# Kernel optimization log

Measured on AMD Instinct MI355X. Metric: run time of the kernel, lower is better.

Reference implementation:

```python
import jax, jax.numpy as jnp
import numpy as np

E, B, T = 7, 50, 100               # ensemble (network_size), no_batches=50, time blocks
D, A, L, H, C = 128, 32, 256, 1024, 128  # data, action, latent, hidden, context sizes
H_STEP = 0.1                        # (t1 - t0) / T == dt -> one SDE step per block


def setup_inputs() -> dict:
    key = jax.random.key(0)
    ks = iter(jax.random.split(key, 64))
    def nrm(shape, scale=1.0):
        return jax.random.normal(next(ks), shape, jnp.float32) * scale
    def ens(i, o):
        s = 1.0 / np.sqrt(i)
        return nrm((E, i, o), s), nrm((E, o), s)
    def lin(i, o):
        s = 1.0 / np.sqrt(i)
        return nrm((i, o), s), nrm((o,), s)
    inp = {}
    inp["enc_w1"], inp["enc_b1"] = ens(D, H)
    inp["enc_w2"], inp["enc_b2"] = ens(H, H)
    inp["enc_w3"], inp["enc_b3"] = ens(H, C)
    inp["qz0_w"], inp["qz0_b"] = ens(C, 2 * L)
    inp["act_w"], inp["act_b"] = ens(L + A + D, L)
    inp["proj_w1"], inp["proj_b1"] = ens(L, H)
    inp["proj_w2"], inp["proj_b2"] = ens(H, H)
    inp["proj_w3"], inp["proj_b3"] = ens(H, D)
    inp["f_w1"], inp["f_b1"] = lin(L, H)
    inp["f_w2"], inp["f_b2"] = lin(H, H)
    inp["f_w3"], inp["f_b3"] = lin(H, L)
    inp["h_w1"], inp["h_b1"] = lin(L, H)
    inp["h_w2"], inp["h_b2"] = lin(H, H)
    inp["h_w3"], inp["h_b3"] = lin(H, L)
    # per-latent-dim g nets: Linear(1,H) -> ReLU -> Linear(H,1), stacked over L dims
    inp["g_w1"] = nrm((L, H), 0.2)
    inp["g_b1"] = nrm((L, H), 0.2)
    inp["g_w2"] = nrm((L, H), 0.2 / np.sqrt(H))
    inp["g_b2"] = 0.5 + nrm((L,), 0.01)   # keep diffusion bounded away from 0
    inp["pz0_mean"] = jnp.zeros((E, 1, L), jnp.float32)
    inp["pz0_logstd"] = jnp.zeros((E, 1, L), jnp.float32)
    inp["xs"] = nrm((E, T * B, D))
    inp["actions"] = nrm((E, T * B, A))
    inp["eps_z0"] = nrm((T, E, B, L))      # torch.randn_like noise for z0 reparam
    inp["dw_noise"] = nrm((T, E * B, L))   # Brownian increment noise (unit std)
    return inp


def reference(enc_w1, enc_b1, enc_w2, enc_b2, enc_w3, enc_b3,
              qz0_w, qz0_b, act_w, act_b,
              proj_w1, proj_b1, proj_w2, proj_b2, proj_w3, proj_b3,
              f_w1, f_b1, f_w2, f_b2, f_w3, f_b3,
              h_w1, h_b1, h_w2, h_b2, h_w3, h_b3,
              g_w1, g_b1, g_w2, g_b2,
              pz0_mean, pz0_logstd,
              xs, actions, eps_z0, dw_noise):
    def ens_lin(x, w, b):  # EnsembleFC: bmm + bias
        return jnp.einsum('ebi,eio->ebo', x, w) + b[:, None, :]

    def encoder(x):
        x = jax.nn.relu(ens_lin(x, enc_w1, enc_b1))
        x = jax.nn.relu(ens_lin(x, enc_w2, enc_b2))
        return ens_lin(x, enc_w3, enc_b3)

    def projector(z):
        z = jnp.tanh(ens_lin(z, proj_w1, proj_b1))
        z = jnp.tanh(ens_lin(z, proj_w2, proj_b2))
        return ens_lin(z, proj_w3, proj_b3)

    def mlp(y, w1, b1, w2, b2, w3, b3):  # Linear-ReLU-Linear-Tanh-Linear
        y = jax.nn.relu(y @ w1 + b1)
        y = jnp.tanh(y @ w2 + b2)
        return y @ w3 + b3

    def g_fn(y):  # vectorized per-dim tiny MLPs: y (N, L) -> (N, L)
        hh = jax.nn.relu(y[:, :, None] * g_w1[None] + g_b1[None])  # (N, L, H)
        return jnp.sum(hh * g_w2[None], axis=-1) + g_b2

    xs_t = jnp.moveaxis(xs.reshape(E, T, B, D), 1, 0)        # (T, E, B, D)
    act_t = jnp.moveaxis(actions.reshape(E, T, B, A), 1, 0)  # (T, E, B, A)
    sqrt_h = jnp.sqrt(jnp.float32(H_STEP))

    def step(carry, inps):
        zs_last, i = carry
        x_i, a_i, eps_i, dw_i = inps
        ctx = encoder(x_i)                                  # (E, B, C)
        q = ens_lin(ctx, qz0_w, qz0_b)                      # (E, B, 2L)
        qm, ql = q[..., :L], q[..., L:]
        z0 = qm + jnp.exp(ql) * eps_i
        z_in = jnp.where(i == 0, z0, zs_last)               # first step uses z0
        lad = jnp.concatenate([z_in, a_i, x_i], axis=2)
        z = ens_lin(lad, act_w, act_b).reshape(E * B, L)
        # one SDE step with logqp (f: posterior drift, h: prior drift, g: diffusion)
        fv = mlp(z, f_w1, f_b1, f_w2, f_b2, f_w3, f_b3)
        hv = mlp(z, h_w1, h_b1, h_w2, h_b2, h_w3, h_b3)
        gv = g_fn(z)
        u = (fv - hv) / gv
        lr = 0.5 * jnp.sum(u * u, axis=-1) * H_STEP         # (E*B,) log-ratio increment
        z_new = z + fv * H_STEP + gv * (sqrt_h * dw_i)
        zs_new = z_new.reshape(E, B, L)
        xm = projector(zs_new)                              # (E, B, D)
        # KL(q(z0) || p(z0)) for diagonal Gaussians
        kl = (pz0_logstd - ql) \
             + (jnp.exp(2.0 * ql) + (qm - pz0_mean) ** 2) / (2.0 * jnp.exp(2.0 * pz0_logstd)) \
             - 0.5
        logqp0 = kl.sum(axis=2).mean(axis=1)                # (E,)
        lr_mean = lr.reshape(E, B).mean(axis=1)             # (E,)
        return (zs_new, i + 1), (lr_mean, logqp0, xm)

    init = (jnp.zeros((E, B, L), xs.dtype), jnp.int32(0))
    (_, _), (lrm, lq0, xms) = jax.lax.scan(step, init, (xs_t, act_t, eps_z0, dw_noise))
    logqp_path = lrm.sum(axis=0) + lq0.sum(axis=0)          # (E,)
    predicted_xs = jnp.moveaxis(xms, 0, 1).reshape(E, T * B, D)
    return logqp_path, predicted_xs
```

## Files before the change

kernel.cpp:

```cpp
#include <hip/hip_runtime.h>
#include <hip/hip_bf16.h>
#include <math.h>

#define E_ 7
#define B_ 50
#define T_ 100
#define D_ 128
#define A_ 32
#define L_ 256
#define H_ 1024
#define C_ 128
#define LAD_ 416
#define EB_ 350
#define TB_ 5000
#define SQRTH 0.31622776601683794f

typedef __attribute__((ext_vector_type(8))) short s8v;
typedef __attribute__((ext_vector_type(4))) float f32x4;
typedef __hip_bfloat16 bf16;

struct BG {
  const bf16* A[8];
  const bf16* W[8];
  const float* bias[8];
  float* Cf[8];
  bf16* Cb[8];
};

template<int BM, int ACT, int OUT>
__global__ __launch_bounds__(256)
void bgemm(BG g, int M, int K, int lda, int ldw, int ldc) {
  __shared__ short As[BM * 64];
  __shared__ short Ws[128 * 64];
  const short* Ap = (const short*)g.A[blockIdx.z];
  const short* Wp = (const short*)g.W[blockIdx.z];
  const int bm = blockIdx.x * BM, bn = blockIdx.y * 128;
  const int tid = threadIdx.x;
  const int wv = tid >> 6, lane = tid & 63;
  const int wm0 = (wv >> 1) * (BM / 2), wn0 = (wv & 1) * 64;
  const int l15 = lane & 15, l4 = lane >> 4;
  constexpr int FM = BM / 32;
  constexpr int AI = BM / 32;
  f32x4 acc[FM][4] = {};
  for (int k0 = 0; k0 < K; k0 += 64) {
    s8v av[AI], wvv[4];
#pragma unroll
    for (int i = 0; i < AI; ++i) {
      const int c = tid + i * 256, r = c >> 3, ck = c & 7;
      s8v v = {};
      if (bm + r < M) v = *(const s8v*)(Ap + (size_t)(bm + r) * lda + k0 + ck * 8);
      av[i] = v;
// ... 60 lines not shown
  }
}

__global__ __launch_bounds__(256)
void cvtT_kernel(const float* __restrict__ src, bf16* __restrict__ dst,
                 int K, int N, long ss, long ds) {
  __shared__ float t[32][33];
  src += (size_t)blockIdx.z * ss;
  dst += (size_t)blockIdx.z * ds;
  const int n0 = blockIdx.x * 32, k0 = blockIdx.y * 32;
  const int tx = threadIdx.x & 31, ty = threadIdx.x >> 5;
#pragma unroll
  for (int i = 0; i < 4; ++i)
    t[ty + 8 * i][tx] = src[(size_t)(k0 + ty + 8 * i) * N + n0 + tx];
  __syncthreads();
#pragma unroll
  for (int i = 0; i < 4; ++i)
    dst[(size_t)(n0 + ty + 8 * i) * K + k0 + tx] = __float2bfloat16(t[tx][ty + 8 * i]);
}

struct B4 { bf16 a, b, c, d; };
__global__ __launch_bounds__(256)
void cvt_kernel(const float* __restrict__ s, bf16* __restrict__ d, int n4) {
  const int i = blockIdx.x * 256 + threadIdx.x;
  if (i < n4) {
    const float4 v = ((const float4*)s)[i];
    B4 o = {__float2bfloat16(v.x), __float2bfloat16(v.y),
            __float2bfloat16(v.z), __float2bfloat16(v.w)};
    ((B4*)d)[i] = o;
  }
}

__global__ __launch_bounds__(256)
void act_gemm(const float* __restrict__ zin, int zin_estride,
              const float* __restrict__ actions, const float* __restrict__ xs,
              const float* __restrict__ act_w, const float* __restrict__ act_b,
              float* __restrict__ zout, bf16* __restrict__ zout_bf, int t) {
  __shared__ float As[16][68];
  __shared__ float Bs[16][64];
  const int tid = threadIdx.x;
  const int e = blockIdx.y;
  const int bn = blockIdx.x * 64;
  const int tm = (tid >> 4) << 2;
  const int tn = (tid & 15) << 2;
  const int am = tid >> 2;
  const int ak = (tid & 3) << 2;
  const int bk = tid >> 4;
  const int bn4 = (tid & 15) << 2;
  const float* W = act_w + (size_t)e * LAD_ * L_;
  const float* zin_e = zin + (size_t)e * zin_estride;
  float acc[4][4] = {};
  for (int k0 = 0; k0 < LAD_; k0 += 16) {
    float4 av = make_float4(0.f, 0.f, 0.f, 0.f);
    const int k = k0 + ak;
    if (am < B_) {
      if (k < L_)
        av = *(const float4*)(zin_e + (size_t)am * L_ + k);
      else if (k < L_ + A_)
        av = *(const float4*)(actions + ((size_t)e * TB_ + (size_t)t * B_ + am) * A_ + (k - L_));
      else
        av = *(const float4*)(xs + ((size_t)e * TB_ + (size_t)t * B_ + am) * D_ + (k - L_ - A_));
    }
    const float4 wv = *(const float4*)(W + (size_t)(k0 + bk) * L_ + (bn + bn4));
    __syncthreads();
    As[ak + 0][am] = av.x; As[ak + 1][am] = av.y;
    As[ak + 2][am] = av.z; As[ak + 3][am] = av.w;
    *(float4*)&Bs[bk][bn4] = wv;
    __syncthreads();
#pragma unroll
    for (int kk = 0; kk < 16; ++kk) {
      const float4 a4 = *(const float4*)&As[kk][tm];
      const float4 b4 = *(const float4*)&Bs[kk][tn];
      const float ar[4] = {a4.x, a4.y, a4.z, a4.w};
      const float br[4] = {b4.x, b4.y, b4.z, b4.w};
#pragma unroll
      for (int i = 0; i < 4; ++i)
#pragma unroll
        for (int j = 0; j < 4; ++j)
          acc[i][j] = fmaf(ar[i], br[j], acc[i][j]);
    }
  }
#pragma unroll
  for (int i = 0; i < 4; ++i) {
    const int m = tm + i;
    if (m < B_) {
#pragma unroll
      for (int j = 0; j < 4; ++j) {
        const float v = acc[i][j] + act_b[(size_t)e * L_ + bn + tn + j];
        const size_t idx = ((size_t)e * B_ + m) * L_ + (bn + tn + j);
        zout[idx] = v;
        zout_bf[idx] = __float2bfloat16(v);
      }
    }
  }
}

__global__ __launch_bounds__(256)
void qkl_kernel(const float* __restrict__ ctx, int rows, int row_off, int ctx_estride,
                const float* __restrict__ qw, const float* __restrict__ qb,
                const float* __restrict__ pm, const float* __restrict__ pl,
                const float* __restrict__ eps0, float* __restrict__ z0,
                float* __restrict__ logqp) {
  __shared__ float cx[16][128];
  __shared__ float red[16];
  const int e = blockIdx.y;
  const int r0 = blockIdx.x * 16;
  const int tid = threadIdx.x;
  {
    const int r = tid >> 4, c = (tid & 15) * 8;
    float4 v0 = make_float4(0.f, 0.f, 0.f, 0.f), v1 = v0;
    if (r0 + r < rows) {
      const float* src = ctx + (size_t)e * ctx_estride + (size_t)(r0 + r) * C_ + c;
      v0 = *(const float4*)src;
      v1 = *(const float4*)(src + 4);
    }
    *(float4*)&cx[r][c] = v0;
    *(float4*)&cx[r][c + 4] = v1;
  }
  if (tid < 16) red[tid] = 0.f;
  __syncthreads();
  const int j = tid;
  const float* w = qw + (size_t)e * C_ * 512;
  float am_[16] = {};
  float al_[16] = {};
  for (int k0 = 0; k0 < C_; k0 += 4) {
    float wm[4], wl[4];
#pragma unroll
    for (int q = 0; q < 4; ++q) {
      wm[q] = w[(size_t)(k0 + q) * 512 + j];
      wl[q] = w[(size_t)(k0 + q) * 512 + 256 + j];
    }
#pragma unroll
    for (int r = 0; r < 16; ++r) {
      const float4 cv = *(const float4*)&cx[r][k0];
      const float cc[4] = {cv.x, cv.y, cv.z, cv.w};
#pragma unroll
      for (int q = 0; q < 4; ++q) {
        am_[r] = fmaf(cc[q], wm[q], am_[r]);
        al_[r] = fmaf(cc[q], wl[q], al_[r]);
      }
    }
  }
  const float qbm = qb[(size_t)e * 512 + j];
  const float qbl = qb[(size_t)e * 512 + 256 + j];
  const float pmv = pm[(size_t)e * L_ + j];
  const float plv = pl[(size_t)e * L_ + j];
  const float inv2e = 0.5f * expf(-2.f * plv);
#pragma unroll
  for (int r = 0; r < 16; ++r) {
    float kl = 0.f;
    if (r0 + r < rows) {
      const float qm_ = am_[r] + qbm;
      const float ql_ = al_[r] + qbl;
      const float dm = qm_ - pmv;
      kl = plv - ql_ + (expf(2.f * ql_) + dm * dm) * inv2e - 0.5f;
      const int gi = row_off + r0 + r;
      if (gi < B_) {
        const size_t zi = ((size_t)e * B_ + gi) * L_ + j;
        z0[zi] = qm_ + expf(ql_) * eps0[zi];
      }
    }
    for (int off = 32; off; off >>= 1) kl += __shfl_xor(kl, off, 64);
    if ((tid & 63) == 0) atomicAdd(&red[r], kl);
  }
  __syncthreads();
  if (tid < 16 && r0 + tid < rows) atomicAdd(&logqp[e], red[tid] * (1.0f / B_));
}

__global__ __launch_bounds__(64)
void g_kernel(const float* __restrict__ z, const float* __restrict__ gw1,
              const float* __restrict__ gb1, const float* __restrict__ gw2,
              const float* __restrict__ gb2, float* __restrict__ gv) {
  const int l = blockIdx.x;
  const int r0 = blockIdx.y * 44;
  const int rend = (r0 + 44 < EB_) ? (r0 + 44) : EB_;
  const int lane = threadIdx.x;
  float w1[16], b1[16], w2[16];
#pragma unroll
  for (int i = 0; i < 16; ++i) {
    const int h = lane + i * 64;
    w1[i] = gw1[(size_t)l * H_ + h];
    b1[i] = gb1[(size_t)l * H_ + h];
    w2[i] = gw2[(size_t)l * H_ + h];
  }
  const float g2 = gb2[l];
  for (int r = r0; r < rend; ++r) {
    const float zv = z[(size_t)r * L_ + l];
    float acc = 0.f;
#pragma unroll
    for (int i = 0; i < 16; ++i) {
      float hh = fmaf(zv, w1[i], b1[i]);
      hh = fmaxf(hh, 0.f);
      acc = fmaf(hh, w2[i], acc);
    }
    for (int off = 32; off; off >>= 1) acc += __shfl_xor(acc, off, 64);
    if (lane == 0) gv[(size_t)r * L_ + l] = acc + g2;
  }
}

__global__ __launch_bounds__(256)
void epi_kernel(const float* __restrict__ fvp, const float* __restrict__ fb3,
                const float* __restrict__ hb3, const float* __restrict__ gv,
                const float* __restrict__ z, const float* __restrict__ dw,
                float* __restrict__ zs_all, bf16* __restrict__ zs_bf,
                float* __restrict__ logqp, int t) {
  __shared__ float wsum[4];
  const int r = blockIdx.x;
  const int l = threadIdx.x;
  const int e = r / B_, b = r - e * B_;
  const size_t rl = (size_t)r * L_ + l;
  float fv = fb3[l], hv = hb3[l];
#pragma unroll
  for (int s = 0; s < 4; ++s) {
    fv += fvp[(size_t)s * EB_ * L_ + rl];
    hv += fvp[(size_t)(4 + s) * EB_ * L_ + rl];
  }
  const float gvv = gv[rl];
  const float u = (fv - hv) / gvv;
  float s_ = u * u;
  for (int off = 32; off; off >>= 1) s_ += __shfl_xor(s_, off, 64);
  if ((l & 63) == 0) wsum[l >> 6] = s_;
  __syncthreads();
  if (l == 0) {
    const float tot = wsum[0] + wsum[1] + wsum[2] + wsum[3];
    atomicAdd(&logqp[e], 0.5f * tot * 0.1f * (1.0f / B_));
  }
  const float znew = z[rl] + fv * 0.1f + gvv * (SQRTH * dw[(size_t)t * EB_ * L_ + rl]);
  const size_t oi = (((size_t)e * T_ + t) * B_ + b) * L_ + l;
  zs_all[oi] = znew;
  zs_bf[oi] = __float2bfloat16(znew);
}

__global__ void init_kernel(float* logqp) {
  if (threadIdx.x < E_) logqp[threadIdx.x] = 0.f;
}

extern "C" void kernel_launch(void* const* d_in, const int* in_sizes, int n_in,
                              void* d_out, int out_size, void* d_ws, size_t ws_size,
                              hipStream_t stream) {
  (void)in_sizes; (void)n_in; (void)out_size;
  const float* enc_w1 = (const float*)d_in[0];
  const float* enc_b1 = (const float*)d_in[1];
  const float* enc_w2 = (const float*)d_in[2];
  const float* enc_b2 = (const float*)d_in[3];
  const float* enc_w3 = (const float*)d_in[4];
  const float* enc_b3 = (const float*)d_in[5];
  const float* qz0_w  = (const float*)d_in[6];
  const float* qz0_b  = (const float*)d_in[7];
  const float* act_w  = (const float*)d_in[8];
  const float* act_b  = (const float*)d_in[9];
  const float* proj_w1 = (const float*)d_in[10];
  const float* proj_b1 = (const float*)d_in[11];
  const float* proj_w2 = (const float*)d_in[12];
  const float* proj_b2 = (const float*)d_in[13];
  const float* proj_w3 = (const float*)d_in[14];
  const float* proj_b3 = (const float*)d_in[15];
  const float* f_w1 = (const float*)d_in[16];
  const float* f_b1 = (const float*)d_in[17];
  const float* f_w2 = (const float*)d_in[18];
  const float* f_b2 = (const float*)d_in[19];
  const float* f_w3 = (const float*)d_in[20];
  const float* f_b3 = (const float*)d_in[21];
  const float* h_w1 = (const float*)d_in[22];
  const float* h_b1 = (const float*)d_in[23];
  const float* h_w2 = (const float*)d_in[24];
  const float* h_b2 = (const float*)d_in[25];
  const float* h_w3 = (const float*)d_in[26];
  const float* h_b3 = (const float*)d_in[27];
  const float* g_w1 = (const float*)d_in[28];
  const float* g_b1 = (const float*)d_in[29];
  const float* g_w2 = (const float*)d_in[30];
  const float* g_b2 = (const float*)d_in[31];
  const float* pz0_mean   = (const float*)d_in[32];
  const float* pz0_logstd = (const float*)d_in[33];
  const float* xs      = (const float*)d_in[34];
  const float* actions = (const float*)d_in[35];
  const float* eps_z0  = (const float*)d_in[36];
  const float* dw      = (const float*)d_in[37];

  float* out = (float*)d_out;
  float* logqp = out;
  float* pred = out + E_;

  char* base = (char*)d_ws;
  size_t off = 0;
  auto alloc = [&](size_t bytes) {
    void* p = base + off;
    off = (off + bytes + 255) & ~(size_t)255;
    return p;
  };
  float* zs_all = (float*)alloc((size_t)E_ * T_ * B_ * L_ * 4);
  bf16* zs_bf   = (bf16*)alloc((size_t)E_ * T_ * B_ * L_ * 2);
  float* z0     = (float*)alloc((size_t)E_ * B_ * L_ * 4);
  float* zbuf   = (float*)alloc((size_t)EB_ * L_ * 4);
  bf16* zbuf_bf = (bf16*)alloc((size_t)EB_ * L_ * 2);
  bf16* fh1     = (bf16*)alloc((size_t)2 * EB_ * H_ * 2);
  bf16* fh2     = (bf16*)alloc((size_t)2 * EB_ * H_ * 2);
  float* fvhvp  = (float*)alloc((size_t)8 * EB_ * L_ * 4);
  float* gvb    = (float*)alloc((size_t)EB_ * L_ * 4);
  bf16* xs_bf   = (bf16*)alloc((size_t)E_ * TB_ * D_ * 2);
  bf16* ew1T = (bf16*)alloc((size_t)E_ * D_ * H_ * 2);
  bf16* ew2T = (bf16*)alloc((size_t)E_ * H_ * H_ * 2);
  bf16* ew3T = (bf16*)alloc((size_t)E_ * H_ * C_ * 2);
  bf16* pw1T = (bf16*)alloc((size_t)E_ * L_ * H_ * 2);
  bf16* pw2T = (bf16*)alloc((size_t)E_ * H_ * H_ * 2);
  bf16* pw3T = (bf16*)alloc((size_t)E_ * H_ * D_ * 2);
  bf16* fw1T = (bf16*)alloc((size_t)L_ * H_ * 2);
  bf16* fw2T = (bf16*)alloc((size_t)H_ * H_ * 2);
  bf16* fw3T = (bf16*)alloc((size_t)H_ * L_ * 2);
  bf16* hw1T = (bf16*)alloc((size_t)L_ * H_ * 2);
  bf16* hw2T = (bf16*)alloc((size_t)H_ * H_ * 2);
  bf16* hw3T = (bf16*)alloc((size_t)H_ * L_ * 2);
  const size_t per_row = (size_t)E_ * (H_ * 2 * 2 + C_ * 4);
  size_t remain = (ws_size > off + 4096) ? (ws_size - off - 4096) : 0;
  int CH = (int)(remain / per_row);
  if (CH > 2500) CH = 2500;
  if (CH < 64) CH = 64;
  bf16* bufA = (bf16*)alloc((size_t)E_ * CH * H_ * 2);
  bf16* bufB = (bf16*)alloc((size_t)E_ * CH * H_ * 2);
  float* bufC = (float*)alloc((size_t)E_ * CH * C_ * 4);

  init_kernel<<<dim3(1), dim3(64), 0, stream>>>(logqp);

  const dim3 cb(256);
  cvt_kernel<<<dim3((E_ * TB_ * D_ / 4 + 255) / 256), cb, 0, stream>>>(xs, xs_bf, E_ * TB_ * D_ / 4);
  cvtT_kernel<<<dim3(H_ / 32, D_ / 32, E_), cb, 0, stream>>>(enc_w1, ew1T, D_, H_, (long)D_ * H_, (long)D_ * H_);
  cvtT_kernel<<<dim3(H_ / 32, H_ / 32, E_), cb, 0, stream>>>(enc_w2, ew2T, H_, H_, (long)H_ * H_, (long)H_ * H_);
  cvtT_kernel<<<dim3(C_ / 32, H_ / 32, E_), cb, 0, stream>>>(enc_w3, ew3T, H_, C_, (long)H_ * C_, (long)H_ * C_);
  cvtT_kernel<<<dim3(H_ / 32, L_ / 32, E_), cb, 0, stream>>>(proj_w1, pw1T, L_, H_, (long)L_ * H_, (long)L_ * H_);
  cvtT_kernel<<<dim3(H_ / 32, H_ / 32, E_), cb, 0, stream>>>(proj_w2, pw2T, H_, H_, (long)H_ * H_, (long)H_ * H_);
  cvtT_kernel<<<dim3(D_ / 32, H_ / 32, E_), cb, 0, stream>>>(proj_w3, pw3T, H_, D_, (long)H_ * D_, (long)H_ * D_);
  cvtT_kernel<<<dim3(H_ / 32, L_ / 32, 1), cb, 0, stream>>>(f_w1, fw1T, L_, H_, 0, 0);
  cvtT_kernel<<<dim3(H_ / 32, H_ / 32, 1), cb, 0, stream>>>(f_w2, fw2T, H_, H_, 0, 0);
  cvtT_kernel<<<dim3(L_ / 32, H_ / 32, 1), cb, 0, stream>>>(f_w3, fw3T, H_, L_, 0, 0);
  cvtT_kernel<<<dim3(H_ / 32, L_ / 32, 1), cb, 0, stream>>>(h_w1, hw1T, L_, H_, 0, 0);
  cvtT_kernel<<<dim3(H_ / 32, H_ / 32, 1), cb, 0, stream>>>(h_w2, hw2T, H_, H_, 0, 0);
  cvtT_kernel<<<dim3(L_ / 32, H_ / 32, 1), cb, 0, stream>>>(h_w3, hw3T, H_, L_, 0, 0);

  BG g;
  for (int c = 0; c < TB_; c += CH) {
    const int rows = (TB_ - c < CH) ? (TB_ - c) : CH;
    const int mt = (rows + 127) / 128;
    for (int e = 0; e < E_; ++e) {
      g.A[e] = xs_bf + ((size_t)e * TB_ + c) * D_;
      g.W[e] = ew1T + (size_t)e * D_ * H_;
      g.bias[e] = enc_b1 + (size_t)e * H_;
      g.Cb[e] = bufA + (size_t)e * CH * H_;
    }
    bgemm<128, 1, 1><<<dim3(mt, H_ / 128, E_), 256, 0, stream>>>(g, rows, D_, D_, D_, H_);
    for (int e = 0; e < E_; ++e) {
      g.A[e] = bufA + (size_t)e * CH * H_;
      g.W[e] = ew2T + (size_t)e * H_ * H_;
      g.bias[e] = enc_b2 + (size_t)e * H_;
      g.Cb[e] = bufB + (size_t)e * CH * H_;
    }
    bgemm<128, 1, 1><<<dim3(mt, H_ / 128, E_), 256, 0, stream>>>(g, rows, H_, H_, H_, H_);
    for (int e = 0; e < E_; ++e) {
      g.A[e] = bufB + (size_t)e * CH * H_;
      g.W[e] = ew3T + (size_t)e * H_ * C_;
      g.bias[e] = enc_b3 + (size_t)e * C_;
      g.Cf[e] = bufC + (size_t)e * CH * C_;
    }
    bgemm<128, 0, 0><<<dim3(mt, C_ / 128, E_), 256, 0, stream>>>(g, rows, H_, H_, H_, C_);
    qkl_kernel<<<dim3((rows + 15) / 16, E_), 256, 0, stream>>>(
        bufC, rows, c, CH * C_, qz0_w, qz0_b, pz0_mean, pz0_logstd, eps_z0, z0, logqp);
  }

  for (int t = 0; t < T_; ++t) {
    const float* zin;
    int zes;
    if (t == 0) { zin = z0; zes = B_ * L_; }
    else { zin = zs_all + (size_t)(t - 1) * B_ * L_; zes = T_ * B_ * L_; }
    act_gemm<<<dim3(L_ / 64, E_), 256, 0, stream>>>(zin, zes, actions, xs, act_w, act_b,
                                                    zbuf, zbuf_bf, t);
    g.A[0] = zbuf_bf; g.W[0] = fw1T; g.bias[0] = f_b1; g.Cb[0] = fh1;
    g.A[1] = zbuf_bf; g.W[1] = hw1T; g.bias[1] = h_b1; g.Cb[1] = fh1 + (size_t)EB_ * H_;
    bgemm<64, 1, 1><<<dim3(6, H_ / 128, 2), 256, 0, stream>>>(g, EB_, L_, L_, L_, H_);
    g.A[0] = fh1; g.W[0] = fw2T; g.bias[0] = f_b2; g.Cb[0] = fh2;
    g.A[1] = fh1 + (size_t)EB_ * H_; g.W[1] = hw2T; g.bias[1] = h_b2;
    g.Cb[1] = fh2 + (size_t)EB_ * H_;
    bgemm<64, 2, 1><<<dim3(6, H_ / 128, 2), 256, 0, stream>>>(g, EB_, H_, H_, H_, H_);
    for (int jj = 0; jj < 8; ++jj) {
      const int fb = jj >> 2, s = jj & 3;
      g.A[jj] = fh2 + (size_t)fb * EB_ * H_ + s * 256;
      g.W[jj] = (fb ? hw3T : fw3T) + s * 256;
      g.bias[jj] = nullptr;
      g.Cf[jj] = fvhvp + (size_t)jj * EB_ * L_;
    }
    bgemm<64, 0, 0><<<dim3(6, L_ / 128, 8), 256, 0, stream>>>(g, EB_, 256, H_, H_, L_);
    g_kernel<<<dim3(L_, 8), 64, 0, stream>>>(zbuf, g_w1, g_b1, g_w2, g_b2, gvb);
    epi_kernel<<<dim3(EB_), 256, 0, stream>>>(fvhvp, f_b3, h_b3, gvb, zbuf, dw,
                                              zs_all, zs_bf, logqp, t);
  }

  for (int c = 0; c < TB_; c += CH) {
    const int rows = (TB_ - c < CH) ? (TB_ - c) : CH;
    const int mt = (rows + 127) / 128;
    for (int e = 0; e < E_; ++e) {
      g.A[e] = zs_bf + ((size_t)e * T_ * B_ + c) * L_;
      g.W[e] = pw1T + (size_t)e * L_ * H_;
      g.bias[e] = proj_b1 + (size_t)e * H_;
      g.Cb[e] = bufA + (size_t)e * CH * H_;
    }
    bgemm<128, 2, 1><<<dim3(mt, H_ / 128, E_), 256, 0, stream>>>(g, rows, L_, L_, L_, H_);
    for (int e = 0; e < E_; ++e) {
      g.A[e] = bufA + (size_t)e * CH * H_;
      g.W[e] = pw2T + (size_t)e * H_ * H_;
      g.bias[e] = proj_b2 + (size_t)e * H_;
      g.Cb[e] = bufB + (size_t)e * CH * H_;
    }
    bgemm<128, 2, 1><<<dim3(mt, H_ / 128, E_), 256, 0, stream>>>(g, rows, H_, H_, H_, H_);
    for (int e = 0; e < E_; ++e) {
      g.A[e] = bufB + (size_t)e * CH * H_;
      g.W[e] = pw3T + (size_t)e * H_ * D_;
      g.bias[e] = proj_b3 + (size_t)e * D_;
      g.Cf[e] = pred + ((size_t)e * TB_ + c) * D_;
    }
    bgemm<128, 0, 0><<<dim3(mt, D_ / 128, E_), 256, 0, stream>>>(g, rows, H_, H_, H_, D_);
  }
}
```

Before: 11.16 ms.

## Fuse SDE time-step loop into one persistent cooperative kernel with grid barriers

```diff
diff --git a/kernel.cpp b/kernel.cpp
--- a/kernel.cpp
+++ b/kernel.cpp
@@ -10,13 +10,14 @@
 #define L_ 256
 #define H_ 1024
 #define C_ 128
-#define LAD_ 416
 #define EB_ 350
 #define TB_ 5000
 #define SQRTH 0.31622776601683794f
+#define NWG 256
 
 typedef __attribute__((ext_vector_type(8))) short s8v;
 typedef __attribute__((ext_vector_type(4))) float f32x4;
+typedef _Float16 f16x2 __attribute__((ext_vector_type(2)));
 typedef __hip_bfloat16 bf16;
 
 struct BG {
@@ -143,75 +144,50 @@
 }
 
 __global__ __launch_bounds__(256)
-void act_gemm(const float* __restrict__ zin, int zin_estride,
-              const float* __restrict__ actions, const float* __restrict__ xs,
-              const float* __restrict__ act_w, const float* __restrict__ act_b,
-              float* __restrict__ zout, bf16* __restrict__ zout_bf, int t) {
-  __shared__ float As[16][68];
-  __shared__ float Bs[16][64];
-  const int tid = threadIdx.x;
-  const int e = blockIdx.y;
-  const int bn = blockIdx.x * 64;
-  const int tm = (tid >> 4) << 2;
-  const int tn = (tid & 15) << 2;
-  const int am = tid >> 2;
-  const int ak = (tid & 3) << 2;
-  const int bk = tid >> 4;
-  const int bn4 = (tid & 15) << 2;
-  const float* W = act_w + (size_t)e * LAD_ * L_;
-  const float* zin_e = zin + (size_t)e * zin_estride;
-  float acc[4][4] = {};
-  for (int k0 = 0; k0 < LAD_; k0 += 16) {
-    float4 av = make_float4(0.f, 0.f, 0.f, 0.f);
-    const int k = k0 + ak;
-    if (am < B_) {
-      if (k < L_)
-        av = *(const float4*)(zin_e + (size_t)am * L_ + k);
-      else if (k < L_ + A_)
-        av = *(const float4*)(actions + ((size_t)e * TB_ + (size_t)t * B_ + am) * A_ + (k - L_));
-      else
-        av = *(const float4*)(xs + ((size_t)e * TB_ + (size_t)t * B_ + am) * D_ + (k - L_ - A_));
-    }
-    const float4 wv = *(const float4*)(W + (size_t)(k0 + bk) * L_ + (bn + bn4));
-    __syncthreads();
-    As[ak + 0][am] = av.x; As[ak + 1][am] = av.y;
-    As[ak + 2][am] = av.z; As[ak + 3][am] = av.w;
-    *(float4*)&Bs[bk][bn4] = wv;
-    __syncthreads();
-#pragma unroll
-    for (int kk = 0; kk < 16; ++kk) {
-      const float4 a4 = *(const float4*)&As[kk][tm];
-      const float4 b4 = *(const float4*)&Bs[kk][tn];
-      const float ar[4] = {a4.x, a4.y, a4.z, a4.w};
-      const float br[4] = {b4.x, b4.y, b4.z, b4.w};
-#pragma unroll
-      for (int i = 0; i < 4; ++i)
-#pragma unroll
-        for (int j = 0; j < 4; ++j)
-          acc[i][j] = fmaf(ar[i], br[j], acc[i][j]);
-    }
-  }
-#pragma unroll
-  for (int i = 0; i < 4; ++i) {
-    const int m = tm + i;
-    if (m < B_) {
-#pragma unroll
-      for (int j = 0; j < 4; ++j) {
-        const float v = acc[i][j] + act_b[(size_t)e * L_ + bn + tn + j];
-        const size_t idx = ((size_t)e * B_ + m) * L_ + (bn + tn + j);
-        zout[idx] = v;
-        zout_bf[idx] = __float2bfloat16(v);
-      }
-    }
-  }
+void ax_build(const float* __restrict__ actions, const float* __restrict__ xs,
+              bf16* __restrict__ dst) {
+  const int idx = blockIdx.x * 256 + threadIdx.x;
+  if (idx >= E_ * TB_ * 192) return;
+  const int k = idx % 192;
+  const int r = (idx / 192) % TB_;
+  const int e = idx / (192 * TB_);
+  float v = 0.f;
+  if (k < 32) v = actions[((size_t)e * TB_ + r) * A_ + k];
+  else if (k < 160) v = xs[((size_t)e * TB_ + r) * D_ + (k - 32)];
+  dst[idx] = __float2bfloat16(v);
+}
+
+__global__ __launch_bounds__(256)
+void waxT_build(const float* __restrict__ act_w, bf16* __restrict__ dst) {
+  const int idx = blockIdx.x * 256 + threadIdx.x;
+  if (idx >= E_ * 256 * 192) return;
+  const int k = idx % 192;
+  const int n = (idx / 192) % 256;
+  const int e = idx / (192 * 256);
+  float v = (k < 160) ? act_w[(size_t)e * 416 * 256 + (size_t)(256 + k) * 256 + n] : 0.f;
+  dst[idx] = __float2bfloat16(v);
+}
+
+__global__ __launch_bounds__(256)
+void wsplitT_build(const float* __restrict__ act_w, bf16* __restrict__ hi,
+                   bf16* __restrict__ lo) {
+  const int idx = blockIdx.x * 256 + threadIdx.x;
+  if (idx >= E_ * 256 * 256) return;
+  const int k = idx & 255;
+  const int n = (idx >> 8) & 255;
+  const int e = idx >> 16;
+  const float w = act_w[(size_t)e * 416 * 256 + (size_t)k * 256 + n];
+  const bf16 h = __float2bfloat16(w);
+  hi[idx] = h;
+  lo[idx] = __float2bfloat16(w - __bfloat162float(h));
 }
 
 __global__ __launch_bounds__(256)
 void qkl_kernel(const float* __restrict__ ctx, int rows, int row_off, int ctx_estride,
                 const float* __restrict__ qw, const float* __restrict__ qb,
                 const float* __restrict__ pm, const float* __restrict__ pl,
-                const float* __restrict__ eps0, float* __restrict__ z0,
-                float* __restrict__ logqp) {
+                const float* __restrict__ eps0, bf16* __restrict__ z0hi,
+                bf16* __restrict__ z0lo, float* __restrict__ logqp) {
   __shared__ float cx[16][128];
   __shared__ float red[16];
   const int e = blockIdx.y;
@@ -268,7 +244,10 @@
       const int gi = row_off + r0 + r;
       if (gi < B_) {
         const size_t zi = ((size_t)e * B_ + gi) * L_ + j;
-        z0[zi] = qm_ + expf(ql_) * eps0[zi];
+        const float z0 = qm_ + expf(ql_) * eps0[zi];
+        const bf16 h = __float2bfloat16(z0);
+        z0hi[zi] = h;
+        z0lo[zi] = __float2bfloat16(z0 - __bfloat162float(h));
       }
     }
     for (int off = 32; off; off >>= 1) kl += __shfl_xor(kl, off, 64);
@@ -278,72 +257,454 @@
   if (tid < 16 && r0 + tid < rows) atomicAdd(&logqp[e], red[tid] * (1.0f / B_));
 }
 
-__global__ __launch_bounds__(64)
-void g_kernel(const float* __restrict__ z, const float* __restrict__ gw1,
-              const float* __restrict__ gb1, const float* __restrict__ gw2,
-              const float* __restrict__ gb2, float* __restrict__ gv) {
-  const int l = blockIdx.x;
-  const int r0 = blockIdx.y * 44;
-  const int rend = (r0 + 44 < EB_) ? (r0 + 44) : EB_;
-  const int lane = threadIdx.x;
-  float w1[16], b1[16], w2[16];
-#pragma unroll
-  for (int i = 0; i < 16; ++i) {
-    const int h = lane + i * 64;
-    w1[i] = gw1[(size_t)l * H_ + h];
-    b1[i] = gb1[(size_t)l * H_ + h];
-    w2[i] = gw2[(size_t)l * H_ + h];
-  }
-  const float g2 = gb2[l];
-  for (int r = r0; r < rend; ++r) {
-    const float zv = z[(size_t)r * L_ + l];
+struct ScanArgs {
+  bf16* zhi; bf16* zlo;
+  float* zP; bf16* zPb;
+  bf16* fh1; bf16* fh2;
+  float* gv;
+  const float* axw;
+  const bf16 *WzhiT, *WzloT;
+  const bf16 *fw1T, *hw1T, *fw2T, *hw2T, *fw3T, *hw3T;
+  const float *fb1, *hb1, *fb2, *hb2, *fb3, *hb3;
+  const float *gw1, *gb1, *gw2, *gb2;
+  const float* dw;
+  float* logqp;
+  bf16* zs_bf;
+  unsigned* bar;
+  int* gctr;
+};
+
+__device__ __forceinline__ void gsync(unsigned* bar, unsigned& ph, int tid) {
+  __threadfence();
+  __syncthreads();
+  ++ph;
+  if (tid == 0) {
+    atomicAdd(bar, 1u);
+    const unsigned tgt = ph * (unsigned)NWG;
+    while (__hip_atomic_load(bar, __ATOMIC_RELAXED, __HIP_MEMORY_SCOPE_AGENT) < tgt)
+      __builtin_amdgcn_s_sleep(2);
+  }
+  __syncthreads();
+  __threadfence();
+}
+
+__device__ void p1_gemm(const ScanArgs& a, int wg, int tid, int t, char* smem) {
+  short* Ahi = (short*)smem;
+  short* Alo = Ahi + 4096;
+  short* Whi = Alo + 4096;
+  short* Wlo = Whi + 4096;
+  const int e = wg >> 2, nt = wg & 3;
+  const int nbase = nt * 64;
+  const short* zh = (const short*)a.zhi + (size_t)e * 50 * 256;
+  const short* zl = (const short*)a.zlo + (size_t)e * 50 * 256;
+  const short* wh = (const short*)a.WzhiT + (size_t)e * 65536 + (size_t)nbase * 256;
+  const short* wl = (const short*)a.WzloT + (size_t)e * 65536 + (size_t)nbase * 256;
+  const int wv = tid >> 6, lane = tid & 63, l15 = lane & 15, l4 = lane >> 4;
+  const int wm0 = (wv >> 1) * 32, wn0 = (wv & 1) * 32;
+  f32x4 acc[2][2] = {};
+  for (int k0 = 0; k0 < 256; k0 += 64) {
+    s8v vah[2], val[2], vwh[2], vwl[2];
+#pragma unroll
+    for (int i = 0; i < 2; ++i) {
+      const int c = tid + i * 256, r = c >> 3, ck = c & 7;
+      vah[i] = {}; val[i] = {};
+      if (r < 50) {
+        vah[i] = *(const s8v*)(zh + (size_t)r * 256 + k0 + ck * 8);
+        val[i] = *(const s8v*)(zl + (size_t)r * 256 + k0 + ck * 8);
+      }
+      vwh[i] = *(const s8v*)(wh + (size_t)r * 256 + k0 + ck * 8);
+      vwl[i] = *(const s8v*)(wl + (size_t)r * 256 + k0 + ck * 8);
+    }
+    __syncthreads();
+#pragma unroll
+    for (int i = 0; i < 2; ++i) {
+      const int c = tid + i * 256, r = c >> 3;
+      const int sw = ((c & 7) ^ (r & 7)) << 3;
+      *(s8v*)(Ahi + r * 64 + sw) = vah[i];
+      *(s8v*)(Alo + r * 64 + sw) = val[i];
+      *(s8v*)(Whi + r * 64 + sw) = vwh[i];
+      *(s8v*)(Wlo + r * 64 + sw) = vwl[i];
+    }
+    __syncthreads();
+#pragma unroll
+    for (int ks = 0; ks < 2; ++ks) {
+      const int ck = ks * 4 + l4;
+      s8v ah[2], al[2], bh[2], bl[2];
+#pragma unroll
+      for (int m = 0; m < 2; ++m) {
+        const int r = wm0 + m * 16 + l15;
+        const int sw = (ck ^ (r & 7)) << 3;
+        ah[m] = *(const s8v*)(Ahi + r * 64 + sw);
+        al[m] = *(const s8v*)(Alo + r * 64 + sw);
+      }
+#pragma unroll
+      for (int n = 0; n < 2; ++n) {
+        const int r = wn0 + n * 16 + l15;
+        const int sw = (ck ^ (r & 7)) << 3;
+        bh[n] = *(const s8v*)(Whi + r * 64 + sw);
+        bl[n] = *(const s8v*)(Wlo + r * 64 + sw);
+      }
+#pragma unroll
+      for (int m = 0; m < 2; ++m)
+#pragma unroll
+        for (int n = 0; n < 2; ++n) {
+          acc[m][n] = __builtin_amdgcn_mfma_f32_16x16x32_bf16(ah[m], bh[n], acc[m][n], 0, 0, 0);
+          acc[m][n] = __builtin_amdgcn_mfma_f32_16x16x32_bf16(al[m], bh[n], acc[m][n], 0, 0, 0);
+          acc[m][n] = __builtin_amdgcn_mfma_f32_16x16x32_bf16(ah[m], bl[n], acc[m][n], 0, 0, 0);
+        }
+    }
+    __syncthreads();
+  }
+#pragma unroll
+  for (int n = 0; n < 2; ++n) {
+    const int col = nbase + wn0 + n * 16 + l15;
+#pragma unroll
+    for (int m = 0; m < 2; ++m)
+#pragma unroll
+      for (int j = 0; j < 4; ++j) {
+        const int row = wm0 + m * 16 + l4 * 4 + j;
+        if (row < 50) {
+          const float zv = acc[m][n][j] +
+              a.axw[((size_t)e * TB_ + t * 50 + row) * 256 + col];
+          const size_t rl = ((size_t)e * 50 + row) * 256 + col;
+          a.zP[rl] = zv;
+          a.zPb[rl] = __float2bfloat16(zv);
+        }
+      }
+  }
+}
+
+__device__ void p2_gemm(const ScanArgs& a, int wg, int tid, char* smem) {
+  short* As = (short*)smem;
+  short* Ws = (short*)smem + 4096;
+  const int mt = wg >> 4, ntile = wg & 15;
+  const int fb = ntile >> 3, nn = ntile & 7;
+  const short* Ap = (const short*)a.zPb;
+  const short* Wp = (const short*)(fb ? a.hw1T : a.fw1T) + (size_t)nn * 128 * 256;
+  const int bm = mt * 64;
+  const int wv = tid >> 6, lane = tid & 63, l15 = lane & 15, l4 = lane >> 4;
+  const int wm0 = (wv >> 1) * 32, wn0 = (wv & 1) * 64;
+  f32x4 acc[2][4] = {};
+  for (int k0 = 0; k0 < 256; k0 += 64) {
+    s8v av[2], wvv[4];
+#pragma unroll
+    for (int i = 0; i < 2; ++i) {
+      const int c = tid + i * 256, r = c >> 3, ck = c & 7;
+      av[i] = {};
+      if (bm + r < EB_) av[i] = *(const s8v*)(Ap + (size_t)(bm + r) * 256 + k0 + ck * 8);
+    }
+#pragma unroll
+    for (int i = 0; i < 4; ++i) {
+      const int c = tid + i * 256, r = c >> 3, ck = c & 7;
+      wvv[i] = *(const s8v*)(Wp + (size_t)r * 256 + k0 + ck * 8);
+    }
+    __syncthreads();
+#pragma unroll
+    for (int i = 0; i < 2; ++i) {
+      const int c = tid + i * 256, r = c >> 3;
+      *(s8v*)(As + r * 64 + (((c & 7) ^ (r & 7)) << 3)) = av[i];
+    }
+#pragma unroll
+    for (int i = 0; i < 4; ++i) {
+      const int c = tid + i * 256, r = c >> 3;
+      *(s8v*)(Ws + r * 64 + (((c & 7) ^ (r & 7)) << 3)) = wvv[i];
+    }
+    __syncthreads();
+#pragma unroll
+    for (int ks = 0; ks < 2; ++ks) {
+      const int ck = ks * 4 + l4;
+      s8v af[2], bfr[4];
+#pragma unroll
+      for (int m = 0; m < 2; ++m) {
+        const int r = wm0 + m * 16 + l15;
+        af[m] = *(const s8v*)(As + r * 64 + ((ck ^ (r & 7)) << 3));
+      }
+#pragma unroll
+      for (int n = 0; n < 4; ++n) {
+        const int r = wn0 + n * 16 + l15;
+        bfr[n] = *(const s8v*)(Ws + r * 64 + ((ck ^ (r & 7)) << 3));
+      }
+#pragma unroll
+      for (int m = 0; m < 2; ++m)
+#pragma unroll
+        for (int n = 0; n < 4; ++n)
+          acc[m][n] = __builtin_amdgcn_mfma_f32_16x16x32_bf16(af[m], bfr[n], acc[m][n], 0, 0, 0);
+    }
+    __syncthreads();
+  }
+  const float* bias = fb ? a.hb1 : a.fb1;
+  bf16* C = a.fh1 + (size_t)fb * EB_ * 1024;
+#pragma unroll
+  for (int n = 0; n < 4; ++n) {
+    const int col = nn * 128 + wn0 + n * 16 + l15;
+    const float bv = bias[col];
+#pragma unroll
+    for (int m = 0; m < 2; ++m)
+#pragma unroll
+      for (int j = 0; j < 4; ++j) {
+        const int row = bm + wm0 + m * 16 + l4 * 4 + j;
+        if (row < EB_)
+          C[(size_t)row * 1024 + col] = __float2bfloat16(fmaxf(acc[m][n][j] + bv, 0.f));
+      }
+  }
+}
+
+__device__ void p3_gemm(const ScanArgs& a, int wg, int tid, char* smem) {
+  short* As = (short*)smem;
+  short* Ws = (short*)smem + 4096;
+  const int mt = wg >> 5, ntile = wg & 31;
+  const int fb = ntile >> 4, nn = ntile & 15;
+  const short* Ap = (const short*)a.fh1 + (size_t)fb * EB_ * 1024;
+  const short* Wp = (const short*)(fb ? a.hw2T : a.fw2T) + (size_t)nn * 64 * 1024;
+  const int bm = mt * 64;
+  const int wv = tid >> 6, lane = tid & 63, l15 = lane & 15, l4 = lane >> 4;
+  const int wm0 = (wv >> 1) * 32, wn0 = (wv & 1) * 32;
+  f32x4 acc[2][2] = {};
+  for (int k0 = 0; k0 < 1024; k0 += 64) {
+    s8v av[2], wvv[2];
+#pragma unroll
+    for (int i = 0; i < 2; ++i) {
+      const int c = tid + i * 256, r = c >> 3, ck = c & 7;
+      av[i] = {};
+      if (bm + r < EB_) av[i] = *(const s8v*)(Ap + (size_t)(bm + r) * 1024 + k0 + ck * 8);
+      wvv[i] = *(const s8v*)(Wp + (size_t)r * 1024 + k0 + ck * 8);
+    }
+    __syncthreads();
+#pragma unroll
+    for (int i = 0; i < 2; ++i) {
+      const int c = tid + i * 256, r = c >> 3;
+      const int sw = ((c & 7) ^ (r & 7)) << 3;
+      *(s8v*)(As + r * 64 + sw) = av[i];
+      *(s8v*)(Ws + r * 64 + sw) = wvv[i];
+    }
+    __syncthreads();
+#pragma unroll
+    for (int ks = 0; ks < 2; ++ks) {
+      const int ck = ks * 4 + l4;
+      s8v af[2], bfr[2];
+#pragma unroll
+      for (int m = 0; m < 2; ++m) {
+        const int r = wm0 + m * 16 + l15;
+        af[m] = *(const s8v*)(As + r * 64 + ((ck ^ (r & 7)) << 3));
+      }
+#pragma unroll
+      for (int n = 0; n < 2; ++n) {
+        const int r = wn0 + n * 16 + l15;
+        bfr[n] = *(const s8v*)(Ws + r * 64 + ((ck ^ (r & 7)) << 3));
+      }
+#pragma unroll
+      for (int m = 0; m < 2; ++m)
+#pragma unroll
+        for (int n = 0; n < 2; ++n)
+          acc[m][n] = __builtin_amdgcn_mfma_f32_16x16x32_bf16(af[m], bfr[n], acc[m][n], 0, 0, 0);
+    }
+    __syncthreads();
+  }
+  const float* bias = fb ? a.hb2 : a.fb2;
+  bf16* C = a.fh2 + (size_t)fb * EB_ * 1024;
+#pragma unroll
+  for (int n = 0; n < 2; ++n) {
+    const int col = nn * 64 + wn0 + n * 16 + l15;
+    const float bv = bias[col];
+#pragma unroll
+    for (int m = 0; m < 2; ++m)
+#pragma unroll
+      for (int j = 0; j < 4; ++j) {
+        const int row = bm + wm0 + m * 16 + l4 * 4 + j;
+        if (row < EB_)
+          C[(size_t)row * 1024 + col] = __float2bfloat16(tanhf(acc[m][n][j] + bv));
+      }
+  }
+}
+
+__device__ void p45(const ScanArgs& a, int wg, int tid, int t, char* smem) {
+  short* Af = (short*)smem;
+  short* Ah = Af + 2048;
+  short* Wf = Ah + 2048;
+  short* Wh = Wf + 4096;
+  const int rt = wg >> 2, lt = wg & 3;
+  const int r0 = rt * 32, lc = lt * 64;
+  const short* Apf = (const short*)a.fh2;
+  const short* Aph = (const short*)a.fh2 + (size_t)EB_ * 1024;
+  const int wv = tid >> 6, lane = tid & 63, l15 = lane & 15, l4 = lane >> 4;
+  const int wn0 = wv * 16;
+  f32x4 aF[2] = {}, aH[2] = {};
+  for (int k0 = 0; k0 < 1024; k0 += 64) {
+    s8v vaf, vah, vwf[2], vwh[2];
+    {
+      const int c = tid, r = c >> 3, ck = c & 7;
+      vaf = {}; vah = {};
+      if (r0 + r < EB_) {
+        vaf = *(const s8v*)(Apf + (size_t)(r0 + r) * 1024 + k0 + ck * 8);
+        vah = *(const s8v*)(Aph + (size_t)(r0 + r) * 1024 + k0 + ck * 8);
+      }
+    }
+#pragma unroll
+    for (int i = 0; i < 2; ++i) {
+      const int c = tid + i * 256, r = c >> 3, ck = c & 7;
+      vwf[i] = *(const s8v*)((const short*)a.fw3T + (size_t)(lc + r) * 1024 + k0 + ck * 8);
+      vwh[i] = *(const s8v*)((const short*)a.hw3T + (size_t)(lc + r) * 1024 + k0 + ck * 8);
+    }
+    __syncthreads();
+    {
+      const int c = tid, r = c >> 3;
+      const int sw = ((c & 7) ^ (r & 7)) << 3;
+      *(s8v*)(Af + r * 64 + sw) = vaf;
+      *(s8v*)(Ah + r * 64 + sw) = vah;
+    }
+#pragma unroll
+    for (int i = 0; i < 2; ++i) {
+      const int c = tid + i * 256, r = c >> 3;
+      const int sw = ((c & 7) ^ (r & 7)) << 3;
+      *(s8v*)(Wf + r * 64 + sw) = vwf[i];
+      *(s8v*)(Wh + r * 64 + sw) = vwh[i];
+    }
+    __syncthreads();
+#pragma unroll
+    for (int ks = 0; ks < 2; ++ks) {
+      const int ck = ks * 4 + l4;
+      const int rb = wn0 + l15;
+      const int swb = (ck ^ (rb & 7)) << 3;
+      s8v bf_ = *(const s8v*)(Wf + rb * 64 + swb);
+      s8v bh_ = *(const s8v*)(Wh + rb * 64 + swb);
+#pragma unroll
+      for (int m = 0; m < 2; ++m) {
+        const int ar = m * 16 + l15;
+        const int swa = (ck ^ (ar & 7)) << 3;
+        s8v af_ = *(const s8v*)(Af + ar * 64 + swa);
+        s8v ah_ = *(const s8v*)(Ah + ar * 64 + swa);
+        aF[m] = __builtin_amdgcn_mfma_f32_16x16x32_bf16(af_, bf_, aF[m], 0, 0, 0);
+        aH[m] = __builtin_amdgcn_mfma_f32_16x16x32_bf16(ah_, bh_, aH[m], 0, 0, 0);
+      }
+    }
+    __syncthreads();
+  }
+  const int col = lc + wn0 + l15;
+  const float fb3v = a.fb3[col];
+  const float hb3v = a.hb3[col];
+  const int e0 = r0 / 50;
+  const int e1 = (r0 + 31) / 50;
+  float s0 = 0.f, s1 = 0.f;
+#pragma unroll
+  for (int m = 0; m < 2; ++m)
+#pragma unroll
+    for (int j = 0; j < 4; ++j) {
+      const int row = r0 + m * 16 + l4 * 4 + j;
+      if (row < EB_) {
+        const float fv = aF[m][j] + fb3v;
+        const float hv = aH[m][j] + hb3v;
+        const size_t rl = (size_t)row * 256 + col;
+        const float gvv = a.gv[rl];
+        const float u = (fv - hv) / gvv;
+        const int e = row / 50;
+        ((e == e0) ? s0 : s1) += u * u;
+        const float znew = a.zP[rl] + 0.1f * fv + gvv * (SQRTH * a.dw[(size_t)t * 89600 + rl]);
+        const bf16 h = __float2bfloat16(znew);
+        a.zhi[rl] = h;
+        a.zlo[rl] = __float2bfloat16(znew - __bfloat162float(h));
+        const int b = row - e * 50;
+        a.zs_bf[(((size_t)e * T_ + t) * B_ + b) * 256 + col] = h;
+      }
+    }
+#pragma unroll
+  for (int o = 32; o; o >>= 1) {
+    s0 += __shfl_xor(s0, o, 64);
+    s1 += __shfl_xor(s1, o, 64);
+  }
+  if (lane == 0) {
+    atomicAdd(&a.logqp[e0], 1e-3f * s0);
+    if (e1 != e0) atomicAdd(&a.logqp[e1], 1e-3f * s1);
+  }
+}
+
+__device__ void g_unit(const ScanArgs& a, int u, int tid) {
+  const int l = u >> 1, hf = u & 1;
+  const int wv = tid >> 6, lane = tid & 63;
+  f16x2 w1h[8], b1h[8], w2h[8];
+  {
+    const float4* q1 = (const float4*)(a.gw1 + (size_t)l * 1024 + lane * 16);
+    const float4* q2 = (const float4*)(a.gb1 + (size_t)l * 1024 + lane * 16);
+    const float4* q3 = (const float4*)(a.gw2 + (size_t)l * 1024 + lane * 16);
+#pragma unroll
+    for (int q = 0; q < 4; ++q) {
+      const float4 v1 = q1[q], v2 = q2[q], v3 = q3[q];
+      w1h[2 * q] = f16x2{(_Float16)v1.x, (_Float16)v1.y};
+      w1h[2 * q + 1] = f16x2{(_Float16)v1.z, (_Float16)v1.w};
+      b1h[2 * q] = f16x2{(_Float16)v2.x, (_Float16)v2.y};
+      b1h[2 * q + 1] = f16x2{(_Float16)v2.z, (_Float16)v2.w};
+      w2h[2 * q] = f16x2{(_Float16)v3.x, (_Float16)v3.y};
+      w2h[2 * q + 1] = f16x2{(_Float16)v3.z, (_Float16)v3.w};
+    }
+  }
+  const float gb2v = a.gb2[l];
+  const f16x2 zz = {};
+  const int rbeg = hf * 176 + wv * 44;
+  int rend = hf * 176 + (wv + 1) * 44;
+  if (rend > EB_) rend = EB_;
+  for (int r = rbeg; r < rend; ++r) {
+    const float zf = a.zP[(size_t)r * 256 + l];
+    const _Float16 zh = (_Float16)zf;
+    const f16x2 z2 = {zh, zh};
     float acc = 0.f;
 #pragma unroll
-    for (int i = 0; i < 16; ++i) {
-      float hh = fmaf(zv, w1[i], b1[i]);
-      hh = fmaxf(hh, 0.f);
-      acc = fmaf(hh, w2[i], acc);
-    }
-    for (int off = 32; off; off >>= 1) acc += __shfl_xor(acc, off, 64);
-    if (lane == 0) gv[(size_t)r * L_ + l] = acc + g2;
-  }
-}
-
-__global__ __launch_bounds__(256)
-void epi_kernel(const float* __restrict__ fvp, const float* __restrict__ fb3,
-                const float* __restrict__ hb3, const float* __restrict__ gv,
-                const float* __restrict__ z, const float* __restrict__ dw,
-                float* __restrict__ zs_all, bf16* __restrict__ zs_bf,
-                float* __restrict__ logqp, int t) {
-  __shared__ float wsum[4];
-  const int r = blockIdx.x;
-  const int l = threadIdx.x;
-  const int e = r / B_, b = r - e * B_;
-  const size_t rl = (size_t)r * L_ + l;
-  float fv = fb3[l], hv = hb3[l];
-#pragma unroll
-  for (int s = 0; s < 4; ++s) {
-    fv += fvp[(size_t)s * EB_ * L_ + rl];
-    hv += fvp[(size_t)(4 + s) * EB_ * L_ + rl];
-  }
-  const float gvv = gv[rl];
-  const float u = (fv - hv) / gvv;
-  float s_ = u * u;
-  for (int off = 32; off; off >>= 1) s_ += __shfl_xor(s_, off, 64);
-  if ((l & 63) == 0) wsum[l >> 6] = s_;
-  __syncthreads();
-  if (l == 0) {
-    const float tot = wsum[0] + wsum[1] + wsum[2] + wsum[3];
-    atomicAdd(&logqp[e], 0.5f * tot * 0.1f * (1.0f / B_));
-  }
-  const float znew = z[rl] + fv * 0.1f + gvv * (SQRTH * dw[(size_t)t * EB_ * L_ + rl]);
-  const size_t oi = (((size_t)e * T_ + t) * B_ + b) * L_ + l;
-  zs_all[oi] = znew;
-  zs_bf[oi] = __float2bfloat16(znew);
-}
-
-__global__ void init_kernel(float* logqp) {
+    for (int i = 0; i < 8; ++i) {
+      f16x2 tt = z2 * w1h[i] + b1h[i];
+#if __has_builtin(__builtin_elementwise_max)
+      tt = __builtin_elementwise_max(tt, zz);
+#else
+      tt[0] = tt[0] > (_Float16)0 ? tt[0] : (_Float16)0;
+      tt[1] = tt[1] > (_Float16)0 ? tt[1] : (_Float16)0;
+#endif
+#if __has_builtin(__builtin_amdgcn_fdot2)
+      acc = __builtin_amdgcn_fdot2(tt, w2h[i], acc, false);
+#else
+      acc += (float)tt[0] * (float)w2h[i][0] + (float)tt[1] * (float)w2h[i][1];
+#endif
+    }
+#pragma unroll
+    for (int o = 32; o; o >>= 1) acc += __shfl_xor(acc, o, 64);
+    if (lane == 0) a.gv[(size_t)r * 256 + l] = acc + gb2v;
+  }
+}
+
+__global__ __launch_bounds__(256, 1) void scan_kernel(ScanArgs a) {
+  __shared__ __align__(16) char smem[32768];
+  __shared__ int s_u;
+  const int wg = blockIdx.x, tid = threadIdx.x;
+  unsigned ph = 0;
+  for (int t = 0; t < T_; ++t) {
+    if (wg == 60 && tid == 0)
+      __hip_atomic_store(a.gctr, 0, __ATOMIC_RELAXED, __HIP_MEMORY_SCOPE_AGENT);
+    if (wg < 28) p1_gemm(a, wg, tid, t, smem);
+    gsync(a.bar, ph, tid);
+    if (wg < 96) p2_gemm(a, wg, tid, smem);
+    for (;;) {
+      if (tid == 0) s_u = atomicAdd(a.gctr, 1);
+      __syncthreads();
+      const int u = s_u;
+      __syncthreads();
+      if (u >= 512) break;
+      g_unit(a, u, tid);
+    }
+    gsync(a.bar, ph, tid);
+    if (wg < 192) p3_gemm(a, wg, tid, smem);
+    for (;;) {
+      if (tid == 0) s_u = atomicAdd(a.gctr, 1);
+      __syncthreads();
+      const int u = s_u;
+      __syncthreads();
+      if (u >= 512) break;
+      g_unit(a, u, tid);
+    }
+    gsync(a.bar, ph, tid);
+    if (wg < 44) p45(a, wg, tid, t, smem);
+    gsync(a.bar, ph, tid);
+  }
+}
+
+__global__ void init_kernel(float* logqp, unsigned* bar, int* gctr) {
   if (threadIdx.x < E_) logqp[threadIdx.x] = 0.f;
+  if (threadIdx.x == 63) { *bar = 0u; *gctr = 0; }
 }
 
 extern "C" void kernel_launch(void* const* d_in, const int* in_sizes, int n_in,
@@ -400,16 +761,20 @@
     off = (off + bytes + 255) & ~(size_t)255;
     return p;
   };
-  float* zs_all = (float*)alloc((size_t)E_ * T_ * B_ * L_ * 4);
-  bf16* zs_bf   = (bf16*)alloc((size_t)E_ * T_ * B_ * L_ * 2);
-  float* z0     = (float*)alloc((size_t)E_ * B_ * L_ * 4);
-  float* zbuf   = (float*)alloc((size_t)EB_ * L_ * 4);
-  bf16* zbuf_bf = (bf16*)alloc((size_t)EB_ * L_ * 2);
-  bf16* fh1     = (bf16*)alloc((size_t)2 * EB_ * H_ * 2);
-  bf16* fh2     = (bf16*)alloc((size_t)2 * EB_ * H_ * 2);
-  float* fvhvp  = (float*)alloc((size_t)8 * EB_ * L_ * 4);
-  float* gvb    = (float*)alloc((size_t)EB_ * L_ * 4);
-  bf16* xs_bf   = (bf16*)alloc((size_t)E_ * TB_ * D_ * 2);
+  bf16* zhi    = (bf16*)alloc((size_t)EB_ * 256 * 2);
+  bf16* zlo    = (bf16*)alloc((size_t)EB_ * 256 * 2);
+  float* zP    = (float*)alloc((size_t)EB_ * 256 * 4);
+  bf16* zPb    = (bf16*)alloc((size_t)EB_ * 256 * 2);
+  bf16* fh1    = (bf16*)alloc((size_t)2 * EB_ * 1024 * 2);
+  bf16* fh2    = (bf16*)alloc((size_t)2 * EB_ * 1024 * 2);
+  float* gvb   = (float*)alloc((size_t)EB_ * 256 * 4);
+  bf16* zs_bf  = (bf16*)alloc((size_t)E_ * T_ * B_ * 256 * 2);
+  float* axw   = (float*)alloc((size_t)E_ * TB_ * 256 * 4);
+  bf16* ax_bf  = (bf16*)alloc((size_t)E_ * TB_ * 192 * 2);
+  bf16* waxT   = (bf16*)alloc((size_t)E_ * 256 * 192 * 2);
+  bf16* WzhiT  = (bf16*)alloc((size_t)E_ * 256 * 256 * 2);
+  bf16* WzloT  = (bf16*)alloc((size_t)E_ * 256 * 256 * 2);
+  bf16* xs_bf  = (bf16*)alloc((size_t)E_ * TB_ * D_ * 2);
   bf16* ew1T = (bf16*)alloc((size_t)E_ * D_ * H_ * 2);
   bf16* ew2T = (bf16*)alloc((size_t)E_ * H_ * H_ * 2);
   bf16* ew3T = (bf16*)alloc((size_t)E_ * H_ * C_ * 2);
@@ -422,6 +787,8 @@
   bf16* hw1T = (bf16*)alloc((size_t)L_ * H_ * 2);
   bf16* hw2T = (bf16*)alloc((size_t)H_ * H_ * 2);
   bf16* hw3T = (bf16*)alloc((size_t)H_ * L_ * 2);
+  unsigned* bar = (unsigned*)alloc(256);
+  int* gctr = (int*)alloc(256);
   const size_t per_row = (size_t)E_ * (H_ * 2 * 2 + C_ * 4);
   size_t remain = (ws_size > off + 4096) ? (ws_size - off - 4096) : 0;
   int CH = (int)(remain / per_row);
@@ -431,7 +798,7 @@
   bf16* bufB = (bf16*)alloc((size_t)E_ * CH * H_ * 2);
   float* bufC = (float*)alloc((size_t)E_ * CH * C_ * 4);
 
-  init_kernel<<<dim3(1), dim3(64), 0, stream>>>(logqp);
+  init_kernel<<<dim3(1), dim3(64), 0, stream>>>(logqp, bar, gctr);
 
   const dim3 cb(256);
   cvt_kernel<<<dim3((E_ * TB_ * D_ / 4 + 255) / 256), cb, 0, stream>>>(xs, xs_bf, E_ * TB_ * D_ / 4);
@@ -447,8 +814,19 @@
   cvtT_kernel<<<dim3(H_ / 32, L_ / 32, 1), cb, 0, stream>>>(h_w1, hw1T, L_, H_, 0, 0);
   cvtT_kernel<<<dim3(H_ / 32, H_ / 32, 1), cb, 0, stream>>>(h_w2, hw2T, H_, H_, 0, 0);
   cvtT_kernel<<<dim3(L_ / 32, H_ / 32, 1), cb, 0, stream>>>(h_w3, hw3T, H_, L_, 0, 0);
+  ax_build<<<dim3((E_ * TB_ * 192 + 255) / 256), cb, 0, stream>>>(actions, xs, ax_bf);
+  waxT_build<<<dim3((E_ * 256 * 192 + 255) / 256), cb, 0, stream>>>(act_w, waxT);
+  wsplitT_build<<<dim3((E_ * 256 * 256 + 255) / 256), cb, 0, stream>>>(act_w, WzhiT, WzloT);
 
   BG g;
+  for (int e = 0; e < E_; ++e) {
+    g.A[e] = ax_bf + (size_t)e * TB_ * 192;
+    g.W[e] = waxT + (size_t)e * 256 * 192;
+    g.bias[e] = act_b + (size_t)e * 256;
+    g.Cf[e] = axw + (size_t)e * TB_ * 256;
+  }
+  bgemm<128, 0, 0><<<dim3((TB_ + 127) / 128, 2, E_), 256, 0, stream>>>(g, TB_, 192, 192, 192, 256);
+
   for (int c = 0; c < TB_; c += CH) {
     const int rows = (TB_ - c < CH) ? (TB_ - c) : CH;
     const int mt = (rows + 127) / 128;
@@ -474,34 +852,24 @@
     }
     bgemm<128, 0, 0><<<dim3(mt, C_ / 128, E_), 256, 0, stream>>>(g, rows, H_, H_, H_, C_);
     qkl_kernel<<<dim3((rows + 15) / 16, E_), 256, 0, stream>>>(
-        bufC, rows, c, CH * C_, qz0_w, qz0_b, pz0_mean, pz0_logstd, eps_z0, z0, logqp);
-  }
-
-  for (int t = 0; t < T_; ++t) {
-    const float* zin;
-    int zes;
-    if (t == 0) { zin = z0; zes = B_ * L_; }
-    else { zin = zs_all + (size_t)(t - 1) * B_ * L_; zes = T_ * B_ * L_; }
-    act_gemm<<<dim3(L_ / 64, E_), 256, 0, stream>>>(zin, zes, actions, xs, act_w, act_b,
-                                                    zbuf, zbuf_bf, t);
-    g.A[0] = zbuf_bf; g.W[0] = fw1T; g.bias[0] = f_b1; g.Cb[0] = fh1;
-    g.A[1] = zbuf_bf; g.W[1] = hw1T; g.bias[1] = h_b1; g.Cb[1] = fh1 + (size_t)EB_ * H_;
-    bgemm<64, 1, 1><<<dim3(6, H_ / 128, 2), 256, 0, stream>>>(g, EB_, L_, L_, L_, H_);
-    g.A[0] = fh1; g.W[0] = fw2T; g.bias[0] = f_b2; g.Cb[0] = fh2;
-    g.A[1] = fh1 + (size_t)EB_ * H_; g.W[1] = hw2T; g.bias[1] = h_b2;
-    g.Cb[1] = fh2 + (size_t)EB_ * H_;
-    bgemm<64, 2, 1><<<dim3(6, H_ / 128, 2), 256, 0, stream>>>(g, EB_, H_, H_, H_, H_);
-    for (int jj = 0; jj < 8; ++jj) {
-      const int fb = jj >> 2, s = jj & 3;
-      g.A[jj] = fh2 + (size_t)fb * EB_ * H_ + s * 256;
-      g.W[jj] = (fb ? hw3T : fw3T) + s * 256;
-      g.bias[jj] = nullptr;
-      g.Cf[jj] = fvhvp + (size_t)jj * EB_ * L_;
-    }
-    bgemm<64, 0, 0><<<dim3(6, L_ / 128, 8), 256, 0, stream>>>(g, EB_, 256, H_, H_, L_);
-    g_kernel<<<dim3(L_, 8), 64, 0, stream>>>(zbuf, g_w1, g_b1, g_w2, g_b2, gvb);
-    epi_kernel<<<dim3(EB_), 256, 0, stream>>>(fvhvp, f_b3, h_b3, gvb, zbuf, dw,
-                                              zs_all, zs_bf, logqp, t);
+        bufC, rows, c, CH * C_, qz0_w, qz0_b, pz0_mean, pz0_logstd, eps_z0,
+        zhi, zlo, logqp);
+  }
+
+  ScanArgs sa;
+  sa.zhi = zhi; sa.zlo = zlo; sa.zP = zP; sa.zPb = zPb;
+  sa.fh1 = fh1; sa.fh2 = fh2; sa.gv = gvb; sa.axw = axw;
+  sa.WzhiT = WzhiT; sa.WzloT = WzloT;
+  sa.fw1T = fw1T; sa.hw1T = hw1T; sa.fw2T = fw2T; sa.hw2T = hw2T;
+  sa.fw3T = fw3T; sa.hw3T = hw3T;
+  sa.fb1 = f_b1; sa.hb1 = h_b1; sa.fb2 = f_b2; sa.hb2 = h_b2;
+  sa.fb3 = f_b3; sa.hb3 = h_b3;
+  sa.gw1 = g_w1; sa.gb1 = g_b1; sa.gw2 = g_w2; sa.gb2 = g_b2;
+  sa.dw = dw; sa.logqp = logqp; sa.zs_bf = zs_bf; sa.bar = bar; sa.gctr = gctr;
+  void* params[] = {(void*)&sa};
+  if (hipLaunchCooperativeKernel((const void*)scan_kernel, dim3(NWG), dim3(256),
+                                 params, 0, stream) != hipSuccess) {
+    scan_kernel<<<dim3(NWG), dim3(256), 0, stream>>>(sa);
   }
 
   for (int c = 0; c < TB_; c += CH) {
```

After: 26.87 ms. +140.7%, slower.
